# Kernel tuning notes

Hardware: AMD Instinct MI355X
Metric: run time of the kernel (lower is better)

## Reference

```python
import jax, jax.numpy as jnp
import numpy as np

DIM = 2048
N_HEADS = 16
HEAD_DIM = 128
KV_HEADS = 1
ROPE_BASE = 10000.0


def _rope_tables(T, dim, dtype):
    inv_freq = 1.0 / (ROPE_BASE ** (jnp.arange(0, dim, 2, dtype=jnp.float32) / dim))
    t = jnp.arange(T, dtype=jnp.float32)
    freqs = jnp.einsum('i,j->ij', t, inv_freq)          # [T, dim/2]
    emb = jnp.concatenate([freqs, freqs], axis=-1)      # [T, dim]
    cos = jnp.cos(emb)[None, None, :, :].astype(dtype)  # [1,1,T,dim]
    sin = jnp.sin(emb)[None, None, :, :].astype(dtype)
    return cos, sin


def _rotate_half(x):
    x1, x2 = jnp.split(x, 2, axis=-1)
    return jnp.concatenate([-x2, x1], axis=-1)


def setup_inputs() -> dict:
    key = jax.random.key(0)
    k1, k2, k3, k4, k5 = jax.random.split(key, 5)
    B, T = 2, 2048
    x = jax.random.normal(k1, (B, T, DIM), dtype=jnp.float32)
    # additive causal mask: 0 on/below diagonal, -1e9 above
    causal = jnp.triu(jnp.full((T, T), -1e9, dtype=jnp.float32), k=1)
    attn_mask = causal[None, None, :, :]
    s = 1.0 / np.sqrt(DIM)
    wq = jax.random.normal(k2, (DIM, N_HEADS * HEAD_DIM), dtype=jnp.float32) * s
    wk = jax.random.normal(k3, (DIM, KV_HEADS * HEAD_DIM), dtype=jnp.float32) * s
    wv = jax.random.normal(k4, (DIM, KV_HEADS * HEAD_DIM), dtype=jnp.float32) * s
    wo = jax.random.normal(k5, (N_HEADS * HEAD_DIM, DIM), dtype=jnp.float32) * s
    return {"x": x, "attn_mask": attn_mask, "wq": wq, "wk": wk, "wv": wv, "wo": wo}


def reference(x, attn_mask, wq, wk, wv, wo):
    B, T, C = x.shape
    q = (x @ wq).reshape(B, T, N_HEADS, HEAD_DIM).transpose(0, 2, 1, 3)   # [B,H,T,d]
    k = (x @ wk).reshape(B, T, KV_HEADS, HEAD_DIM).transpose(0, 2, 1, 3)  # [B,1,T,d]
    v = (x @ wv).reshape(B, T, KV_HEADS, HEAD_DIM).transpose(0, 2, 1, 3)  # [B,1,T,d]
    cos, sin = _rope_tables(T, HEAD_DIM, x.dtype)
    q = q * cos + _rotate_half(q) * sin
    k = k * cos + _rotate_half(k) * sin
    # KV head broadcasts over the H dim inside matmul (MQA expand path)
    att = jnp.matmul(q, k.swapaxes(-1, -2)) / np.sqrt(HEAD_DIM)          # [B,H,T,T]
    att = att + attn_mask
    w = jax.nn.softmax(att, axis=-1)
    y = jnp.matmul(w, v)                                                  # [B,H,T,d]
    y = y.transpose(0, 2, 1, 3).reshape(B, T, N_HEADS * HEAD_DIM)
    y = y @ wo
    k_exp = jnp.broadcast_to(k, (B, N_HEADS, T, HEAD_DIM))
    v_exp = jnp.broadcast_to(v, (B, N_HEADS, T, HEAD_DIM))
    return y, k_exp, v_exp
```

## Files before the change

### kernel.cpp

```cpp
#include <hip/hip_runtime.h>
#include <hip/hip_bf16.h>
#include <cstdint>
#include <cstddef>

#define B_SZ   2
#define T_SEQ  2048
#define C_DIM  2048
#define NH     16
#define HD     128

typedef __attribute__((ext_vector_type(8))) short s8v;
typedef __attribute__((ext_vector_type(4))) float f32x4;

typedef __attribute__((address_space(3))) char lds_char;
typedef __attribute__((address_space(1))) const char glob_char;

__device__ __forceinline__ unsigned short f2bf(float f) {
    union { float f; uint32_t i; } v; v.f = f;
    uint32_t r = (v.i + 0x7FFFu + ((v.i >> 16) & 1u)) >> 16;
    return (unsigned short)r;
}

__device__ __forceinline__ unsigned short cvt1_bf16(float f) {
    unsigned int w;
    asm("v_cvt_pk_bf16_f32 %0, %1, %2" : "=v"(w) : "v"(f), "v"(f));
    return (unsigned short)w;
}

template <int CTRL>
__device__ __forceinline__ float dpp_ror_f(float x) {
    int t = __builtin_amdgcn_update_dpp(__float_as_int(x), __float_as_int(x),
                                        CTRL, 0xf, 0xf, false);
    return __int_as_float(t);
}
__device__ __forceinline__ float rowmax16(float v) {
    v = fmaxf(v, dpp_ror_f<0x121>(v));
    v = fmaxf(v, dpp_ror_f<0x122>(v));
    v = fmaxf(v, dpp_ror_f<0x124>(v));
    v = fmaxf(v, dpp_ror_f<0x128>(v));
    return v;
}

__global__ void k_f32_to_bf16(const float* __restrict__ in,
                              unsigned short* __restrict__ out, int n4) {
    int i = blockIdx.x * blockDim.x + threadIdx.x;
    int stride = gridDim.x * blockDim.x;
    for (; i < n4; i += stride) {
        float4 v = reinterpret_cast<const float4*>(in)[i];
        ushort4 o;
        o.x = f2bf(v.x); o.y = f2bf(v.y); o.z = f2bf(v.z); o.w = f2bf(v.w);
        reinterpret_cast<ushort4*>(out)[i] = o;
    }
}

__global__ void k_transp_bf16(const float* __restrict__ in,
                              unsigned short* __restrict__ out,
                              int R, int C, int ldo) {
    __shared__ unsigned short tile[64][66];
    int x0 = blockIdx.x * 64, y0 = blockIdx.y * 64;
    int tx = threadIdx.x, ty = threadIdx.y;
#pragma unroll
    for (int j = 0; j < 16; ++j) {
        int r = y0 + ty + j * 4;
        tile[ty + j * 4][tx] = f2bf(in[(size_t)r * C + x0 + tx]);
    }
    __syncthreads();
#pragma unroll
    for (int j = 0; j < 16; ++j) {
        int orow = x0 + ty + j * 4;
        out[(size_t)orow * ldo + y0 + tx] = tile[tx][ty + j * 4];
    }
}

__global__ void k_rope_tab(float* __restrict__ cosT, float* __restrict__ sinT) {
    int idx = blockIdx.x * blockDim.x + threadIdx.x;
    if (idx >= T_SEQ * 64) return;
    int t = idx >> 6, i = idx & 63;
    float inv = powf(10000.0f, -(float)i / 64.0f);
    float ang = (float)t * inv;
    cosT[idx] = cosf(ang);
    sinT[idx] = sinf(ang);
}

#define BM 128
#define BN 128
#define BK 64

__global__ __launch_bounds__(256) void k_gemm_bt(
        const unsigned short* __restrict__ A,
        const unsigned short* __restrict__ Bt,
        float* __restrict__ C, int M, int N, int K, int ldc) {
    __shared__ char smem[BM * BK * 2 + BN * BK * 2];
    char* As = smem;
    char* Bs = smem + BM * BK * 2;
    int tid = threadIdx.x, lane = tid & 63, wid = tid >> 6;
    int m0 = blockIdx.y * BM, n0 = blockIdx.x * BN;
    int wr = wid >> 1, wc = wid & 1;

    f32x4 acc[4][4] = {};

    int srow = wid * 32 + (lane >> 3);
    int cp = lane & 7;

    for (int k0 = 0; k0 < K; k0 += BK) {
#pragma unroll
        for (int i = 0; i < 4; ++i) {
            int row = srow + i * 8;
            int c = cp ^ (row & 7);
            const unsigned short* ga = A + (size_t)(m0 + row) * K + k0 + c * 8;
            const unsigned short* gb = Bt + (size_t)(n0 + row) * K + k0 + c * 8;
            __builtin_amdgcn_global_load_lds((glob_char*)ga,
                (lds_char*)(As + wid * 4096 + i * 1024), 16, 0, 0);
            __builtin_amdgcn_global_load_lds((glob_char*)gb,
                (lds_char*)(Bs + wid * 4096 + i * 1024), 16, 0, 0);
        }
        __syncthreads();

#pragma unroll
        for (int kc = 0; kc < 2; ++kc) {
            s8v af[4], bfr[4];
#pragma unroll
            for (int mi = 0; mi < 4; ++mi) {
                int row = wr * 64 + mi * 16 + (lane & 15);
                int slot = (kc * 4 + (lane >> 4)) ^ (row & 7);
                af[mi] = *reinterpret_cast<const s8v*>(As + row * 128 + slot * 16);
            }
#pragma unroll
            for (int ni = 0; ni < 4; ++ni) {
                int row = wc * 64 + ni * 16 + (lane & 15);
                int slot = (kc * 4 + (lane >> 4)) ^ (row & 7);
                bfr[ni] = *reinterpret_cast<const s8v*>(Bs + row * 128 + slot * 16);
            }
#pragma unroll
            for (int mi = 0; mi < 4; ++mi)
#pragma unroll
                for (int ni = 0; ni < 4; ++ni)
                    acc[mi][ni] = __builtin_amdgcn_mfma_f32_16x16x32_bf16(
                        af[mi], bfr[ni], acc[mi][ni], 0, 0, 0);
        }
        __syncthreads();
    }

#pragma unroll
    for (int mi = 0; mi < 4; ++mi) {
        int row = m0 + wr * 64 + mi * 16 + ((lane >> 4) << 2);
#pragma unroll
        for (int ni = 0; ni < 4; ++ni) {
            int col = n0 + wc * 64 + ni * 16 + (lane & 15);
            float* cp2 = C + (size_t)row * ldc + col;
#pragma unroll
            for (int r = 0; r < 4; ++r)
                cp2[(size_t)r * ldc] = acc[mi][ni][r];
        }
    }
}

__global__ void k_qkv_transform(const float* __restrict__ qkv,
                                const float* __restrict__ cosT,
                                const float* __restrict__ sinT,
                                unsigned short* __restrict__ qB,
                                unsigned short* __restrict__ kB,
                                unsigned short* __restrict__ vT,
                                float* __restrict__ kexp,
                                float* __restrict__ vexp) {
    int bt = blockIdx.x;
    int b = bt >> 11, t = bt & 2047;
    int tid = threadIdx.x;
    const float* base = qkv + (size_t)bt * 2304;
    const float SCALE = 0.08838834764831845f * 1.4426950408889634f;

    for (int i = tid; i < 1024; i += 256) {
        int h = i >> 6, d = i & 63;
        float c = cosT[t * 64 + d], s = sinT[t * 64 + d];
        float q1 = base[h * 128 + d], q2 = base[h * 128 + d + 64];
        float o1 = (q1 * c - q2 * s) * SCALE;
        float o2 = (q2 * c + q1 * s) * SCALE;
        size_t qoff = ((size_t)(b * NH + h) * T_SEQ + t) * HD + d;
        qB[qoff] = f2bf(o1);
        qB[qoff + 64] = f2bf(o2);
    }
    if (tid < 64) {
        int d = tid;
        float c = cosT[t * 64 + d], s = sinT[t * 64 + d];
        float k1 = base[2048 + d], k2 = base[2048 + d + 64];
        float o1 = k1 * c - k2 * s;
        float o2 = k2 * c + k1 * s;
        size_t koff = ((size_t)b * T_SEQ + t) * HD + d;
        kB[koff] = f2bf(o1);
        kB[koff + 64] = f2bf(o2);
#pragma unroll
        for (int h = 0; h < NH; ++h) {
            size_t eoff = ((size_t)(b * NH + h) * T_SEQ + t) * HD + d;
            kexp[eoff] = o1;
            kexp[eoff + 64] = o2;
        }
    }
    if (tid >= 128) {
        int d = tid - 128;
        float v = base[2176 + d];
        vT[((size_t)b * HD + d) * T_SEQ + t] = f2bf(v);
#pragma unroll
        for (int h = 0; h < NH; ++h)
            vexp[((size_t)(b * NH + h) * T_SEQ + t) * HD + d] = v;
    }
}

__global__ __launch_bounds__(256, 2) void k_flash_attn(
        const unsigned short* __restrict__ qB,
        const unsigned short* __restrict__ kB,
        const unsigned short* __restrict__ vT,
        unsigned short* __restrict__ yattn) {
    __shared__ char smem[81920];
    int tid = threadIdx.x, lane = tid & 63, wvid = tid >> 6;
    int blk = blockIdx.x;
    int b = blk >> 8;
    int rem = blk & 255;
    int h = rem & 15;
    int jj = rem >> 4;
    int j0 = 16 + jj;
    int j1 = 15 - jj;
    int qrow0[2];
    qrow0[0] = j0 * 64 + wvid * 16;
    qrow0[1] = j1 * 64 + wvid * 16;

    char* Ks0 = smem;
    char* Vs0 = smem + 32768;
    char* pbase = smem + 65536 + wvid * 4096;

    const unsigned short* kbB   = kB + (size_t)b * T_SEQ * HD;
    const unsigned short* vbase = vT + (size_t)b * HD * T_SEQ;

    s8v aq[2][4];
#pragma unroll
    for (int rt = 0; rt < 2; ++rt) {
        const unsigned short* qbase =
            qB + ((size_t)(b * NH + h) * T_SEQ + qrow0[rt]) * HD;
#pragma unroll
        for (int kc = 0; kc < 4; ++kc)
            aq[rt][kc] = *reinterpret_cast<const s8v*>(
                qbase + (size_t)(lane & 15) * HD + kc * 32 + (lane >> 4) * 8);
    }

    float m_r[2][4], l_r[2][4];
#pragma unroll
    for (int rt = 0; rt < 2; ++rt)
#pragma unroll
        for (int r = 0; r < 4; ++r) { m_r[rt][r] = -3e38f; l_r[rt][r] = 0.f; }
    f32x4 o[2][8] = {};

    int NT = j0 + 1;

    auto stage = [&](int buf, int t) {
        int kv0 = t * 64;
#pragma unroll
        for (int j = 0; j < 4; ++j) {
            int n = j * 256 + tid;
            int row = n >> 4, ch = n & 15;
            const unsigned short* src =
                kbB + (size_t)(kv0 + row) * HD + (ch ^ (row & 7)) * 8;
            __builtin_amdgcn_global_load_lds((glob_char*)src,
                (lds_char*)(Ks0 + buf * 16384 + j * 4096 + wvid * 1024), 16, 0, 0);
        }
#pragma unroll
        for (int j = 0; j < 4; ++j) {
            int n = j * 256 + tid;
            int row = n >> 3, ch = n & 7;
            const unsigned short* src =
                vbase + (size_t)row * T_SEQ + kv0 + (ch ^ (row & 7)) * 8;
            __builtin_amdgcn_global_load_lds((glob_char*)src,
                (lds_char*)(Vs0 + buf * 16384 + j * 4096 + wvid * 1024), 16, 0, 0);
        }
    };

    stage(0, 0);
    asm volatile("s_waitcnt vmcnt(0)" ::: "memory");
    __builtin_amdgcn_s_barrier();
    __builtin_amdgcn_sched_barrier(0);

    for (int t = 0; t < NT; ++t) {
        int cur = t & 1;
        if (t + 1 < NT) stage(cur ^ 1, t + 1);
        int kv0 = t * 64;
        const char* Kc = Ks0 + cur * 16384;
        const char* Vc = Vs0 + cur * 16384;
        int act1 = (t <= j1);

        f32x4 sfr[2][4] = {};
        __builtin_amdgcn_s_setprio(1);
#pragma unroll
        for (int kc = 0; kc < 4; ++kc) {
            s8v kf[4];
#pragma unroll
            for (int n = 0; n < 4; ++n) {
                int row = n * 16 + (lane & 15);
                int byte = row * 256 +
                    ((kc * 64 + (lane >> 4) * 16) ^ ((row & 7) << 4));
                kf[n] = *reinterpret_cast<const s8v*>(Kc + byte);
            }
#pragma unroll
            for (int n = 0; n < 4; ++n)
                sfr[0][n] = __builtin_amdgcn_mfma_f32_16x16x32_bf16(
                    aq[0][kc], kf[n], sfr[0][n], 0, 0, 0);
            if (act1) {
#pragma unroll
                for (int n = 0; n < 4; ++n)
                    sfr[1][n] = __builtin_amdgcn_mfma_f32_16x16x32_bf16(
                        aq[1][kc], kf[n], sfr[1][n], 0, 0, 0);
            }
        }
        __builtin_amdgcn_s_setprio(0);

#pragma unroll
        for (int rt = 0; rt < 2; ++rt) {
            if (rt == 1 && !act1) continue;
            if (kv0 + 63 > qrow0[rt]) {
#pragma unroll
                for (int n = 0; n < 4; ++n)
#pragma unroll
                    for (int r = 0; r < 4; ++r) {
                        int col = kv0 + n * 16 + (lane & 15);
                        int row = qrow0[rt] + ((lane >> 4) << 2) + r;
                        if (col > row) sfr[rt][n][r] = -1e9f;
                    }
            }
            float pm[4];
#pragma unroll
            for (int r = 0; r < 4; ++r) {
                float v0 = fmaxf(fmaxf(sfr[rt][0][r], sfr[rt][1][r]),
                                 fmaxf(sfr[rt][2][r], sfr[rt][3][r]));
                pm[r] = rowmax16(v0);
            }
            int ok = (pm[0] <= m_r[rt][0] + 8.0f) &
                     (pm[1] <= m_r[rt][1] + 8.0f) &
                     (pm[2] <= m_r[rt][2] + 8.0f) &
                     (pm[3] <= m_r[rt][3] + 8.0f);
            if (!__all(ok)) {
#pragma unroll
                for (int r = 0; r < 4; ++r) {
                    float mn = fmaxf(m_r[rt][r], pm[r]);
                    float al = exp2f(m_r[rt][r] - mn);
                    l_r[rt][r] *= al;
#pragma unroll
                    for (int ds = 0; ds < 8; ++ds)
                        o[rt][ds][r] *= al;
                    m_r[rt][r] = mn;
                }
            }
#pragma unroll
            for (int n = 0; n < 4; ++n)
#pragma unroll
                for (int r = 0; r < 4; ++r) {
                    float p = exp2f(sfr[rt][n][r] - m_r[rt][r]);
                    sfr[rt][n][r] = p;
                    l_r[rt][r] += p;
                }
        }

#pragma unroll
        for (int rt = 0; rt < 2; ++rt) {
            if (rt == 1 && !act1) continue;
#pragma unroll
            for (int n = 0; n < 4; ++n)
#pragma unroll
                for (int r = 0; r < 4; ++r) {
                    int rowl = rt * 16 + ((lane >> 4) << 2) + r;
                    int byte = rowl * 128 + (n * 16 + (lane & 15)) * 2;
                    byte ^= ((rowl & 7) << 4);
                    *reinterpret_cast<unsigned short*>(pbase + byte) =
                        cvt1_bf16(sfr[rt][n][r]);
                }
        }
        asm volatile("s_waitcnt lgkmcnt(0)" ::: "memory");
        __builtin_amdgcn_sched_barrier(0);

        __builtin_amdgcn_s_setprio(1);
#pragma unroll
        for (int kc2 = 0; kc2 < 2; ++kc2) {
            s8v pa[2];
#pragma unroll
            for (int rt = 0; rt < 2; ++rt) {
                int rowl = rt * 16 + (lane & 15);
                int byte = rowl * 128 +
                    ((kc2 * 64 + (lane >> 4) * 16) ^ ((rowl & 7) << 4));
                pa[rt] = *reinterpret_cast<const s8v*>(pbase + byte);
            }
#pragma unroll
            for (int ds = 0; ds < 8; ++ds) {
                int vrow = ds * 16 + (lane & 15);
                int vbyte = vrow * 128 +
                    ((kc2 * 64 + (lane >> 4) * 16) ^ ((vrow & 7) << 4));
                s8v bv = *reinterpret_cast<const s8v*>(Vc + vbyte);
                o[0][ds] = __builtin_amdgcn_mfma_f32_16x16x32_bf16(
                    pa[0], bv, o[0][ds], 0, 0, 0);
                if (act1)
                    o[1][ds] = __builtin_amdgcn_mfma_f32_16x16x32_bf16(
                        pa[1], bv, o[1][ds], 0, 0, 0);
            }
        }
        __builtin_amdgcn_s_setprio(0);

        asm volatile("s_waitcnt vmcnt(0) lgkmcnt(0)" ::: "memory");
        __builtin_amdgcn_s_barrier();
        __builtin_amdgcn_sched_barrier(0);
    }

#pragma unroll
    for (int rt = 0; rt < 2; ++rt) {
        float inv[4];
#pragma unroll
        for (int r = 0; r < 4; ++r) {
            float lv = l_r[rt][r];
#pragma unroll
            for (int off = 1; off < 16; off <<= 1)
                lv += __shfl_xor(lv, off);
            inv[r] = 1.0f / lv;
        }
#pragma unroll
        for (int ds = 0; ds < 8; ++ds)
#pragma unroll
            for (int r = 0; r < 4; ++r) {
                int row = qrow0[rt] + ((lane >> 4) << 2) + r;
                int col = h * HD + ds * 16 + (lane & 15);
                yattn[((size_t)b * T_SEQ + row) * C_DIM + col] =
                    cvt1_bf16(o[rt][ds][r] * inv[r]);
            }
    }
}

extern "C" void kernel_launch(void* const* d_in, const int* in_sizes, int n_in,
                              void* d_out, int out_size, void* d_ws, size_t ws_size,
                              hipStream_t stream) {
    const float* x  = (const float*)d_in[0];
    const float* wq = (const float*)d_in[2];
    const float* wk = (const float*)d_in[3];
    const float* wv = (const float*)d_in[4];
    const float* wo = (const float*)d_in[5];

    char* ws = (char*)d_ws;
    size_t off = 0;
    auto alloc = [&](size_t bytes) -> void* {
        void* p = ws + off;
        off += (bytes + 255) & ~(size_t)255;
        return p;
    };
    unsigned short* xb   = (unsigned short*)alloc((size_t)4096 * 2048 * 2);
    unsigned short* wT   = (unsigned short*)alloc((size_t)2304 * 2048 * 2);
    unsigned short* woT  = (unsigned short*)alloc((size_t)2048 * 2048 * 2);
    float*          qkv  = (float*)alloc((size_t)4096 * 2304 * 4);
    float*          cosT = (float*)alloc((size_t)2048 * 64 * 4);
    float*          sinT = (float*)alloc((size_t)2048 * 64 * 4);
    unsigned short* qB   = (unsigned short*)alloc((size_t)2 * 16 * 2048 * 128 * 2);
    unsigned short* kB   = (unsigned short*)alloc((size_t)2 * 2048 * 128 * 2);
    unsigned short* vT   = (unsigned short*)alloc((size_t)2 * 128 * 2048 * 2);
    unsigned short* yattn = (unsigned short*)qkv;

    float* y_out = (float*)d_out;
    float* kexp  = y_out + (size_t)2 * 2048 * 2048;
    float* vexp  = kexp + (size_t)2 * 16 * 2048 * 128;

    dim3 tb(64, 4);
    k_f32_to_bf16<<<2048, 256, 0, stream>>>(x, xb, 4096 * 2048 / 4);
    k_transp_bf16<<<dim3(32, 32), tb, 0, stream>>>(wq, wT, 2048, 2048, 2048);
    k_transp_bf16<<<dim3(2, 32), tb, 0, stream>>>(wk, wT + (size_t)2048 * 2048, 2048, 128, 2048);
    k_transp_bf16<<<dim3(2, 32), tb, 0, stream>>>(wv, wT + (size_t)2176 * 2048, 2048, 128, 2048);
    k_transp_bf16<<<dim3(32, 32), tb, 0, stream>>>(wo, woT, 2048, 2048, 2048);
    k_rope_tab<<<512, 256, 0, stream>>>(cosT, sinT);

    k_gemm_bt<<<dim3(2304 / BN, 4096 / BM), 256, 0, stream>>>(
        xb, wT, qkv, 4096, 2304, 2048, 2304);
    k_qkv_transform<<<4096, 256, 0, stream>>>(qkv, cosT, sinT, qB, kB, vT, kexp, vexp);
    k_flash_attn<<<512, 256, 0, stream>>>(qB, kB, vT, yattn);
    k_gemm_bt<<<dim3(2048 / BN, 4096 / BM), 256, 0, stream>>>(
        yattn, woT, y_out, 4096, 2048, 2048, 2048);
}
```

Before: 252.5 us.

## Fuse Q RoPE and scaling into QKV GEMM epilogue, remap GEMM blocks per XCD

```diff
diff --git a/kernel.cpp b/kernel.cpp
--- a/kernel.cpp
+++ b/kernel.cpp
@@ -14,6 +14,8 @@
 
 typedef __attribute__((address_space(3))) char lds_char;
 typedef __attribute__((address_space(1))) const char glob_char;
+
+#define QSCALE 0.12751887f
 
 __device__ __forceinline__ unsigned short f2bf(float f) {
     union { float f; uint32_t i; } v; v.f = f;
@@ -72,14 +74,16 @@
     }
 }
 
-__global__ void k_rope_tab(float* __restrict__ cosT, float* __restrict__ sinT) {
+__global__ void k_rope_tab(float* __restrict__ cosT, float* __restrict__ sinT,
+                           float* __restrict__ cosT2, float* __restrict__ sinT2) {
     int idx = blockIdx.x * blockDim.x + threadIdx.x;
     if (idx >= T_SEQ * 64) return;
     int t = idx >> 6, i = idx & 63;
     float inv = powf(10000.0f, -(float)i / 64.0f);
     float ang = (float)t * inv;
-    cosT[idx] = cosf(ang);
-    sinT[idx] = sinf(ang);
+    float c = cosf(ang), s = sinf(ang);
+    cosT[idx] = c;  sinT[idx] = s;
+    cosT2[i * T_SEQ + t] = c;  sinT2[i * T_SEQ + t] = s;
 }
 
 #define BM 128
@@ -89,12 +93,16 @@
 __global__ __launch_bounds__(256) void k_gemm_bt(
         const unsigned short* __restrict__ A,
         const unsigned short* __restrict__ Bt,
-        float* __restrict__ C, int M, int N, int K, int ldc) {
+        float* __restrict__ C, int M, int N, int K, int ldc, int gx) {
     __shared__ char smem[BM * BK * 2 + BN * BK * 2];
     char* As = smem;
     char* Bs = smem + BM * BK * 2;
     int tid = threadIdx.x, lane = tid & 63, wid = tid >> 6;
-    int m0 = blockIdx.y * BM, n0 = blockIdx.x * BN;
+    int nwg = gridDim.x, cpx = nwg >> 3;
+    int orig = blockIdx.x;
+    int wg = (orig & 7) * cpx + (orig >> 3);
+    int bx = wg % gx, by = wg / gx;
+    int m0 = by * BM, n0 = bx * BN;
     int wr = wid >> 1, wc = wid & 1;
 
     f32x4 acc[4][4] = {};
@@ -155,34 +163,125 @@
     }
 }
 
-__global__ void k_qkv_transform(const float* __restrict__ qkv,
-                                const float* __restrict__ cosT,
-                                const float* __restrict__ sinT,
-                                unsigned short* __restrict__ qB,
-                                unsigned short* __restrict__ kB,
-                                unsigned short* __restrict__ vT,
-                                float* __restrict__ kexp,
-                                float* __restrict__ vexp) {
+__global__ __launch_bounds__(256) void k_gemm_qkv(
+        const unsigned short* __restrict__ A,
+        const unsigned short* __restrict__ Bt,
+        const float* __restrict__ cosT2,
+        const float* __restrict__ sinT2,
+        unsigned short* __restrict__ qB,
+        float* __restrict__ qkvKV) {
+    const int GX = 18, K = 2048;
+    __shared__ char smem[BM * BK * 2 + BN * BK * 2];
+    char* As = smem;
+    char* Bs = smem + BM * BK * 2;
+    int tid = threadIdx.x, lane = tid & 63, wid = tid >> 6;
+    int nwg = gridDim.x, cpx = nwg >> 3;
+    int orig = blockIdx.x;
+    int wg = (orig & 7) * cpx + (orig >> 3);
+    int bx = wg % GX, by = wg / GX;
+    int m0 = by * BM, n0 = bx * BN;
+    int l15 = lane & 15, l4 = lane >> 4;
+
+    f32x4 acc[2][8] = {};
+
+    int srow = wid * 32 + (lane >> 3);
+    int cp = lane & 7;
+
+    for (int k0 = 0; k0 < K; k0 += BK) {
+#pragma unroll
+        for (int i = 0; i < 4; ++i) {
+            int row = srow + i * 8;
+            int c = cp ^ (row & 7);
+            const unsigned short* ga = A + (size_t)(m0 + row) * K + k0 + c * 8;
+            const unsigned short* gb = Bt + (size_t)(n0 + row) * K + k0 + c * 8;
+            __builtin_amdgcn_global_load_lds((glob_char*)ga,
+                (lds_char*)(As + wid * 4096 + i * 1024), 16, 0, 0);
+            __builtin_amdgcn_global_load_lds((glob_char*)gb,
+                (lds_char*)(Bs + wid * 4096 + i * 1024), 16, 0, 0);
+        }
+        __syncthreads();
+
+#pragma unroll
+        for (int kc = 0; kc < 2; ++kc) {
+            s8v af[2], bfr[8];
+#pragma unroll
+            for (int mi = 0; mi < 2; ++mi) {
+                int row = wid * 32 + mi * 16 + l15;
+                int slot = (kc * 4 + l4) ^ (row & 7);
+                af[mi] = *reinterpret_cast<const s8v*>(As + row * 128 + slot * 16);
+            }
+#pragma unroll
+            for (int ni = 0; ni < 8; ++ni) {
+                int row = ni * 16 + l15;
+                int slot = (kc * 4 + l4) ^ (row & 7);
+                bfr[ni] = *reinterpret_cast<const s8v*>(Bs + row * 128 + slot * 16);
+            }
+#pragma unroll
+            for (int mi = 0; mi < 2; ++mi)
+#pragma unroll
+                for (int ni = 0; ni < 8; ++ni)
+                    acc[mi][ni] = __builtin_amdgcn_mfma_f32_16x16x32_bf16(
+                        af[mi], bfr[ni], acc[mi][ni], 0, 0, 0);
+        }
+        __syncthreads();
+    }
+
+    if (bx < 16) {
+        int b = m0 >> 11, h = bx;
+#pragma unroll
+        for (int mi = 0; mi < 2; ++mi) {
+            int t0 = (m0 + wid * 32 + mi * 16 + l4 * 4) & (T_SEQ - 1);
+#pragma unroll
+            for (int nip = 0; nip < 4; ++nip) {
+                int d = nip * 16 + l15;
+                float4 c4 = *reinterpret_cast<const float4*>(cosT2 + (size_t)d * T_SEQ + t0);
+                float4 s4 = *reinterpret_cast<const float4*>(sinT2 + (size_t)d * T_SEQ + t0);
+#pragma unroll
+                for (int r = 0; r < 4; ++r) {
+                    float x1 = acc[mi][nip][r];
+                    float x2 = acc[mi][nip + 4][r];
+                    float cc = (&c4.x)[r], ss = (&s4.x)[r];
+                    float o1 = (x1 * cc - x2 * ss) * QSCALE;
+                    float o2 = (x2 * cc + x1 * ss) * QSCALE;
+                    size_t qoff = ((size_t)(b * NH + h) * T_SEQ + t0 + r) * HD + d;
+                    qB[qoff] = cvt1_bf16(o1);
+                    qB[qoff + 64] = cvt1_bf16(o2);
+                }
+            }
+        }
+    } else {
+        int colb = (bx - 16) * 128;
+#pragma unroll
+        for (int mi = 0; mi < 2; ++mi) {
+            int row = m0 + wid * 32 + mi * 16 + l4 * 4;
+#pragma unroll
+            for (int ni = 0; ni < 8; ++ni) {
+                int col = colb + ni * 16 + l15;
+                float* cp2 = qkvKV + (size_t)row * 256 + col;
+#pragma unroll
+                for (int r = 0; r < 4; ++r)
+                    cp2[(size_t)r * 256] = acc[mi][ni][r];
+            }
+        }
+    }
+}
+
+__global__ void k_kv_transform(const float* __restrict__ qkvKV,
+                               const float* __restrict__ cosT,
+                               const float* __restrict__ sinT,
+                               unsigned short* __restrict__ kB,
+                               unsigned short* __restrict__ vT,
+                               float* __restrict__ kexp,
+                               float* __restrict__ vexp) {
     int bt = blockIdx.x;
     int b = bt >> 11, t = bt & 2047;
     int tid = threadIdx.x;
-    const float* base = qkv + (size_t)bt * 2304;
-    const float SCALE = 0.08838834764831845f * 1.4426950408889634f;
-
-    for (int i = tid; i < 1024; i += 256) {
-        int h = i >> 6, d = i & 63;
-        float c = cosT[t * 64 + d], s = sinT[t * 64 + d];
-        float q1 = base[h * 128 + d], q2 = base[h * 128 + d + 64];
-        float o1 = (q1 * c - q2 * s) * SCALE;
-        float o2 = (q2 * c + q1 * s) * SCALE;
-        size_t qoff = ((size_t)(b * NH + h) * T_SEQ + t) * HD + d;
-        qB[qoff] = f2bf(o1);
-        qB[qoff + 64] = f2bf(o2);
-    }
+    const float* base = qkvKV + (size_t)bt * 256;
+
     if (tid < 64) {
         int d = tid;
         float c = cosT[t * 64 + d], s = sinT[t * 64 + d];
-        float k1 = base[2048 + d], k2 = base[2048 + d + 64];
+        float k1 = base[d], k2 = base[d + 64];
         float o1 = k1 * c - k2 * s;
         float o2 = k2 * c + k1 * s;
         size_t koff = ((size_t)b * T_SEQ + t) * HD + d;
@@ -197,7 +296,7 @@
     }
     if (tid >= 128) {
         int d = tid - 128;
-        float v = base[2176 + d];
+        float v = base[128 + d];
         vT[((size_t)b * HD + d) * T_SEQ + t] = f2bf(v);
 #pragma unroll
         for (int h = 0; h < NH; ++h)
@@ -443,16 +542,18 @@
         off += (bytes + 255) & ~(size_t)255;
         return p;
     };
-    unsigned short* xb   = (unsigned short*)alloc((size_t)4096 * 2048 * 2);
-    unsigned short* wT   = (unsigned short*)alloc((size_t)2304 * 2048 * 2);
-    unsigned short* woT  = (unsigned short*)alloc((size_t)2048 * 2048 * 2);
-    float*          qkv  = (float*)alloc((size_t)4096 * 2304 * 4);
-    float*          cosT = (float*)alloc((size_t)2048 * 64 * 4);
-    float*          sinT = (float*)alloc((size_t)2048 * 64 * 4);
-    unsigned short* qB   = (unsigned short*)alloc((size_t)2 * 16 * 2048 * 128 * 2);
-    unsigned short* kB   = (unsigned short*)alloc((size_t)2 * 2048 * 128 * 2);
-    unsigned short* vT   = (unsigned short*)alloc((size_t)2 * 128 * 2048 * 2);
-    unsigned short* yattn = (unsigned short*)qkv;
+    unsigned short* xb    = (unsigned short*)alloc((size_t)4096 * 2048 * 2);
+    unsigned short* wT    = (unsigned short*)alloc((size_t)2304 * 2048 * 2);
+    unsigned short* woT   = (unsigned short*)alloc((size_t)2048 * 2048 * 2);
+    float*          qkvKV = (float*)alloc((size_t)4096 * 256 * 4);
+    float*          cosT  = (float*)alloc((size_t)2048 * 64 * 4);
+    float*          sinT  = (float*)alloc((size_t)2048 * 64 * 4);
+    float*          cosT2 = (float*)alloc((size_t)64 * 2048 * 4);
+    float*          sinT2 = (float*)alloc((size_t)64 * 2048 * 4);
+    unsigned short* qB    = (unsigned short*)alloc((size_t)2 * 16 * 2048 * 128 * 2);
+    unsigned short* kB    = (unsigned short*)alloc((size_t)2 * 2048 * 128 * 2);
+    unsigned short* vT    = (unsigned short*)alloc((size_t)2 * 128 * 2048 * 2);
+    unsigned short* yattn = (unsigned short*)alloc((size_t)4096 * 2048 * 2);
 
     float* y_out = (float*)d_out;
     float* kexp  = y_out + (size_t)2 * 2048 * 2048;
@@ -464,12 +565,11 @@
     k_transp_bf16<<<dim3(2, 32), tb, 0, stream>>>(wk, wT + (size_t)2048 * 2048, 2048, 128, 2048);
     k_transp_bf16<<<dim3(2, 32), tb, 0, stream>>>(wv, wT + (size_t)2176 * 2048, 2048, 128, 2048);
     k_transp_bf16<<<dim3(32, 32), tb, 0, stream>>>(wo, woT, 2048, 2048, 2048);
-    k_rope_tab<<<512, 256, 0, stream>>>(cosT, sinT);
-
-    k_gemm_bt<<<dim3(2304 / BN, 4096 / BM), 256, 0, stream>>>(
-        xb, wT, qkv, 4096, 2304, 2048, 2304);
-    k_qkv_transform<<<4096, 256, 0, stream>>>(qkv, cosT, sinT, qB, kB, vT, kexp, vexp);
+    k_rope_tab<<<512, 256, 0, stream>>>(cosT, sinT, cosT2, sinT2);
+
+    k_gemm_qkv<<<576, 256, 0, stream>>>(xb, wT, cosT2, sinT2, qB, qkvKV);
+    k_kv_transform<<<4096, 256, 0, stream>>>(qkvKV, cosT, sinT, kB, vT, kexp, vexp);
     k_flash_attn<<<512, 256, 0, stream>>>(qB, kB, vT, yattn);
-    k_gemm_bt<<<dim3(2048 / BN, 4096 / BM), 256, 0, stream>>>(
-        yattn, woT, y_out, 4096, 2048, 2048, 2048);
-}
+    k_gemm_bt<<<512, 256, 0, stream>>>(
+        yattn, woT, y_out, 4096, 2048, 2048, 2048, 16);
+}
```

Result: no change. 249.1 us (median of 2 runs) (-1.4%).
